# Kernel optimization log

Hardware: AMD Instinct MI355X
Metric: run time of the kernel (lower is better)

Reference implementation:

```python
import jax, jax.numpy as jnp
import numpy as np

B, D_IN, J = 65536, 512, 8
HIDDEN = [256, 128, 64]


def setup_inputs() -> dict:
    key = jax.random.key(0)
    ks = jax.random.split(key, 8)
    dims = [D_IN] + HIDDEN
    inp = {
        "x": jax.random.normal(ks[0], (B, D_IN), dtype=jnp.float32),
        # soft domain indicator (one-hot in practice; math is a weighted sum either way)
        "domain_indicator": jax.random.uniform(ks[1], (B, J), dtype=jnp.float32),
    }
    for i in range(3):
        fin, fout = dims[i], dims[i + 1]
        scale = (2.0 / (fin + fout)) ** 0.5  # glorot_normal
        inp[f"sk{i}"] = jax.random.normal(ks[2 + i], (fin, fout), dtype=jnp.float32) * scale
        inp[f"sb{i}"] = jnp.zeros((fout,), dtype=jnp.float32)
        inp[f"dk{i}"] = jax.random.normal(ks[5 + i], (J, fin, fout), dtype=jnp.float32) * scale
        inp[f"db{i}"] = jnp.zeros((J, fout), dtype=jnp.float32)
    return inp


def _star_forward(x, domain_indicator, layers):
    # layer 0: x is [B, D]; fused shared*domain weights -> batched per-domain GEMM
    sk, sb, dk, db = layers[0]
    w = sk[None] * dk                                   # [J, D, H0]
    h = jnp.einsum('bi,jio->bjo', x, w) + (sb[None] + db)[None]  # [B, J, H0]
    h = jax.nn.relu(h)
    for sk, sb, dk, db in layers[1:]:
        w = sk[None] * dk                               # [J, Hi, Hi+1]
        h = jnp.einsum('bji,jio->bjo', h, w) + (sb[None] + db)[None]
        h = jax.nn.relu(h)
    # select/mix domains: sum_j h[b,j,:] * indicator[b,j]
    return jnp.einsum('bjo,bj->bo', h, domain_indicator)


def reference(x, domain_indicator, sk0, sb0, dk0, db0, sk1, sb1, dk1, db1, sk2, sb2, dk2, db2):
    layers = [(sk0, sb0, dk0, db0), (sk1, sb1, dk1, db1), (sk2, sb2, dk2, db2)]
    return _star_forward(x, domain_indicator, layers)
```

## Files before the change

kernel.cpp:

```cpp
#include <hip/hip_runtime.h>
#include <stdint.h>


namespace {

typedef __attribute__((ext_vector_type(8))) short bf16x8;
typedef __attribute__((ext_vector_type(4))) float f32x4;

union Frag { bf16x8 v; unsigned int u[4]; };

constexpr size_t WS_L0   = 0;
constexpr size_t WS_L1   = 4194304;
constexpr size_t WS_L2   = 5242880;
constexpr size_t WS_B0   = 5505024;
constexpr size_t WS_B1   = 5513216;
constexpr size_t WS_B2   = 5517312;
constexpr size_t WS_X    = 5519360;
constexpr size_t WS_TOTAL_BIG = WS_X + (size_t)65536 * 2048;

constexpr int PREP_TOTAL = 1048576 + 262144 + 65536 + 2048 + 1024 + 512;
constexpr int XSPLIT_THREADS = 65536 * 64;

__device__ __forceinline__ void splitpair(float a, float b,
                                          unsigned int& hi, unsigned int& lo) {
    unsigned int ua = __float_as_uint(a);
    unsigned int ub = __float_as_uint(b);
    unsigned int ha = ua & 0xffff0000u;
    unsigned int hb = ub & 0xffff0000u;
    float ra = a - __uint_as_float(ha);
    float rb = b - __uint_as_float(hb);
    hi = (ua >> 16) | hb;
    lo = (__float_as_uint(ra) >> 16) | (__float_as_uint(rb) & 0xffff0000u);
}

__device__ __forceinline__ unsigned int packsplit(float v) {
    unsigned int u = __float_as_uint(v);
    unsigned int h = u & 0xffff0000u;
    float r = v - __uint_as_float(h);
    return h | (__float_as_uint(r) >> 16);
}

__device__ __forceinline__ void unpack2(unsigned int e0, unsigned int e1,
                                        unsigned int& hi, unsigned int& lo) {
    hi = (e0 >> 16) | (e1 & 0xffff0000u);
    lo = (e0 & 0xffffu) | (e1 << 16);
}

__device__ __forceinline__ void unpack2p(unsigned int e0, unsigned int e1,
                                         unsigned int& hi, unsigned int& lo) {
    hi = __builtin_amdgcn_perm(e1, e0, 0x07060302u);
    lo = __builtin_amdgcn_perm(e1, e0, 0x05040100u);
}

__device__ __forceinline__ unsigned int packsplitp(float v) {
    unsigned int u = __float_as_uint(v);
    float r = v - __uint_as_float(u & 0xffff0000u);
    return __builtin_amdgcn_perm(u, __float_as_uint(r), 0x07060302u);
}

__global__ void prep_ws(const float* __restrict__ sk0, const float* __restrict__ dk0,
                        const float* __restrict__ sk1, const float* __restrict__ dk1,
                        const float* __restrict__ sk2, const float* __restrict__ dk2,
                        const float* __restrict__ sb0, const float* __restrict__ db0,
                        const float* __restrict__ sb1, const float* __restrict__ db1,
                        const float* __restrict__ sb2, const float* __restrict__ db2,
                        char* __restrict__ ws) {
    int tid = blockIdx.x * 256 + threadIdx.x;
    if (tid < 1048576) {
        int n = tid & 255, k = (tid >> 8) & 511, j = tid >> 17;
        float wv = sk0[k * 256 + n] * dk0[(size_t)(j * 512 + k) * 256 + n];
        unsigned int u = __float_as_uint(wv);
        unsigned int h = u & 0xffff0000u;
        float r = wv - __uint_as_float(h);
        int pair = (j * 16 + (k >> 5)) * 16 + (n >> 4);
        int lane = (n & 15) | (((k >> 3) & 3) << 4);
        size_t off = WS_L0 + (size_t)pair * 2048 + lane * 16 + (k & 7) * 2;
        *(unsigned short*)(ws + off)        = (unsigned short)(u >> 16);
        *(unsigned short*)(ws + off + 1024) = (unsigned short)(__float_as_uint(r) >> 16);
    } else if (tid < 1310720) {
        int t = tid - 1048576;
        int n = t & 127, k = (t >> 7) & 255, j = t >> 15;
        float wv = sk1[k * 128 + n] * dk1[(size_t)(j * 256 + k) * 128 + n];
        unsigned int u = __float_as_uint(wv);
        unsigned int h = u & 0xffff0000u;
        float r = wv - __uint_as_float(h);
        int pair = (j * 8 + (k >> 5)) * 8 + (n >> 4);
        int lane = (n & 15) | (((k >> 3) & 3) << 4);
        size_t off = WS_L1 + (size_t)pair * 2048 + lane * 16 + (k & 7) * 2;
        *(unsigned short*)(ws + off)        = (unsigned short)(u >> 16);
        *(unsigned short*)(ws + off + 1024) = (unsigned short)(__float_as_uint(r) >> 16);
    } else if (tid < 1376256) {
        int t = tid - 1310720;
        int n = t & 63, k = (t >> 6) & 127, j = t >> 13;
        float wv = sk2[k * 64 + n] * dk2[(size_t)(j * 128 + k) * 64 + n];
        unsigned int u = __float_as_uint(wv);
        unsigned int h = u & 0xffff0000u;
        float r = wv - __uint_as_float(h);
        int pair = (j * 4 + (k >> 5)) * 4 + (n >> 4);
        int lane = (n & 15) | (((k >> 3) & 3) << 4);
        size_t off = WS_L2 + (size_t)pair * 2048 + lane * 16 + (k & 7) * 2;
        *(unsigned short*)(ws + off)        = (unsigned short)(u >> 16);
        *(unsigned short*)(ws + off + 1024) = (unsigned short)(__float_as_uint(r) >> 16);
    } else if (tid < 1378304) {
        int t = tid - 1376256;
        ((float*)(ws + WS_B0))[t] = sb0[t & 255] + db0[t];
    } else if (tid < 1379328) {
        int t = tid - 1378304;
        ((float*)(ws + WS_B1))[t] = sb1[t & 127] + db1[t];
    } else if (tid < PREP_TOTAL) {
        int t = tid - 1379328;
        ((float*)(ws + WS_B2))[t] = sb2[t & 63] + db2[t];
    }
}

__global__ void prep_xsplit(const float* __restrict__ x, char* __restrict__ ws) {
    int t = blockIdx.x * 256 + threadIdx.x;
    if (t >= XSPLIT_THREADS) return;
    const float4 a0 = *(const float4*)(x + (size_t)t * 8);
    const float4 a1 = *(const float4*)(x + (size_t)t * 8 + 4);
    unsigned int hi[4], lo[4];
    splitpair(a0.x, a0.y, hi[0], lo[0]);
    splitpair(a0.z, a0.w, hi[1], lo[1]);
    splitpair(a1.x, a1.y, hi[2], lo[2]);
    splitpair(a1.z, a1.w, hi[3], lo[3]);
    char* dst = ws + WS_X + (size_t)t * 32;
    *(uint4*)dst        = *(uint4*)hi;
    *(uint4*)(dst + 16) = *(uint4*)lo;
}

__global__ __launch_bounds__(512, 4) void star_mfma_v3(
    const float* __restrict__ ind,
    const char* __restrict__ ws,
    float* __restrict__ out)
{
    __shared__ unsigned int H0s[32 * 260];
    __shared__ unsigned int H1s[32 * 132];
    __shared__ float indS[8 * 33];

    const int tid  = threadIdx.x;
    const int w    = tid >> 6;
    const int lane = tid & 63;
    const int c    = lane & 15;
    const int q    = lane >> 4;
    const int b0   = blockIdx.x * 32;
    const int mt2  = w >> 2;
    const int nt2  = w & 3;

    const char* xp  = ws + WS_X;
    const char* wB0 = ws + WS_L0;
    const char* wB1 = ws + WS_L1;
    const char* wB2 = ws + WS_L2;
    const float* bias0 = (const float*)(ws + WS_B0);
    const float* bias1 = (const float*)(ws + WS_B1);
    const float* bias2 = (const float*)(ws + WS_B2);

    if (tid < 256) indS[(tid & 7) * 33 + (tid >> 3)] = ind[(size_t)b0 * 8 + tid];

    const f32x4 z = {0.f, 0.f, 0.f, 0.f};
    f32x4 oacc = z;

    __syncthreads();

    for (int jp = 0; jp < 2; ++jp) {
        f32x4 acc0[4][2][2];
#pragma unroll
        for (int jj = 0; jj < 4; ++jj)
#pragma unroll
            for (int mt = 0; mt < 2; ++mt)
#pragma unroll
                for (int ntl = 0; ntl < 2; ++ntl) acc0[jj][mt][ntl] = z;

        for (int kc = 0; kc < 16; ++kc) {
            Frag Ahi[2], Alo[2];
#pragma unroll
            for (int mt = 0; mt < 2; ++mt) {
                const char* ap = xp + (size_t)(b0 + mt * 16 + c) * 2048 + (kc * 4 + q) * 32;
                *(uint4*)Ahi[mt].u = *(const uint4*)ap;
                *(uint4*)Alo[mt].u = *(const uint4*)(ap + 16);
            }
#pragma unroll
            for (int jj = 0; jj < 4; ++jj) {
                const int j = jp * 4 + jj;
#pragma unroll
                for (int ntl = 0; ntl < 2; ++ntl) {
                    const int nt = w * 2 + ntl;
                    const char* pb = wB0 + ((size_t)((j * 16 + kc) * 16 + nt) * 2048) + lane * 16;
                    Frag Bhi, Blo;
                    *(uint4*)Bhi.u = *(const uint4*)pb;
                    *(uint4*)Blo.u = *(const uint4*)(pb + 1024);
#pragma unroll
                    for (int mt = 0; mt < 2; ++mt) {
                        acc0[jj][mt][ntl] = __builtin_amdgcn_mfma_f32_16x16x32_bf16(Ahi[mt].v, Bhi.v, acc0[jj][mt][ntl], 0, 0, 0);
                        acc0[jj][mt][ntl] = __builtin_amdgcn_mfma_f32_16x16x32_bf16(Ahi[mt].v, Blo.v, acc0[jj][mt][ntl], 0, 0, 0);
                        acc0[jj][mt][ntl] = __builtin_amdgcn_mfma_f32_16x16x32_bf16(Alo[mt].v, Bhi.v, acc0[jj][mt][ntl], 0, 0, 0);
                    }
                }
            }
        }

#pragma unroll
        for (int jj = 0; jj < 4; ++jj) {
            const int j = jp * 4 + jj;

#pragma unroll
            for (int ntl = 0; ntl < 2; ++ntl) {
                const float bv = bias0[j * 256 + w * 32 + ntl * 16 + c];
#pragma unroll
                for (int mt = 0; mt < 2; ++mt)
#pragma unroll
                    for (int r = 0; r < 4; ++r) {
                        float v = fmaxf(acc0[jj][mt][ntl][r] + bv, 0.f);
                        H0s[(mt * 16 + q * 4 + r) * 260 + w * 32 + ntl * 16 + c] = packsplitp(v);
                    }
            }
            __syncthreads();

            f32x4 acc1[2]; acc1[0] = z; acc1[1] = z;
            for (int kc = 0; kc < 8; ++kc) {
                Frag Ahi[2], Alo[2];
#pragma unroll
                for (int mt = 0; mt < 2; ++mt) {
                    const unsigned int* hp = &H0s[(mt * 16 + c) * 260 + kc * 32 + q * 8];
                    uint4 e0 = *(const uint4*)hp;
                    uint4 e1 = *(const uint4*)(hp + 4);
                    unpack2p(e0.x, e0.y, Ahi[mt].u[0], Alo[mt].u[0]);
                    unpack2p(e0.z, e0.w, Ahi[mt].u[1], Alo[mt].u[1]);
                    unpack2p(e1.x, e1.y, Ahi[mt].u[2], Alo[mt].u[2]);
                    unpack2p(e1.z, e1.w, Ahi[mt].u[3], Alo[mt].u[3]);
                }
                const char* pb = wB1 + ((size_t)((j * 8 + kc) * 8 + w) * 2048) + lane * 16;
                Frag Bhi, Blo;
                *(uint4*)Bhi.u = *(const uint4*)pb;
                *(uint4*)Blo.u = *(const uint4*)(pb + 1024);
#pragma unroll
                for (int mt = 0; mt < 2; ++mt) {
                    acc1[mt] = __builtin_amdgcn_mfma_f32_16x16x32_bf16(Ahi[mt].v, Bhi.v, acc1[mt], 0, 0, 0);
                    acc1[mt] = __builtin_amdgcn_mfma_f32_16x16x32_bf16(Ahi[mt].v, Blo.v, acc1[mt], 0, 0, 0);
                    acc1[mt] = __builtin_amdgcn_mfma_f32_16x16x32_bf16(Alo[mt].v, Bhi.v, acc1[mt], 0, 0, 0);
                }
            }
            {
                const float bv = bias1[j * 128 + w * 16 + c];
#pragma unroll
                for (int mt = 0; mt < 2; ++mt)
#pragma unroll
                    for (int r = 0; r < 4; ++r) {
                        float v = fmaxf(acc1[mt][r] + bv, 0.f);
                        H1s[(mt * 16 + q * 4 + r) * 132 + w * 16 + c] = packsplitp(v);
                    }
            }
            __syncthreads();

            f32x4 acc2 = z;
            for (int kc = 0; kc < 4; ++kc) {
                Frag Ahi, Alo;
                const unsigned int* hp = &H1s[(mt2 * 16 + c) * 132 + kc * 32 + q * 8];
                uint4 e0 = *(const uint4*)hp;
                uint4 e1 = *(const uint4*)(hp + 4);
                unpack2p(e0.x, e0.y, Ahi.u[0], Alo.u[0]);
                unpack2p(e0.z, e0.w, Ahi.u[1], Alo.u[1]);
                unpack2p(e1.x, e1.y, Ahi.u[2], Alo.u[2]);
                unpack2p(e1.z, e1.w, Ahi.u[3], Alo.u[3]);
                const char* pb = wB2 + ((size_t)((j * 4 + kc) * 4 + nt2) * 2048) + lane * 16;
                Frag Bhi, Blo;
                *(uint4*)Bhi.u = *(const uint4*)pb;
                *(uint4*)Blo.u = *(const uint4*)(pb + 1024);
                acc2 = __builtin_amdgcn_mfma_f32_16x16x32_bf16(Ahi.v, Bhi.v, acc2, 0, 0, 0);
                acc2 = __builtin_amdgcn_mfma_f32_16x16x32_bf16(Ahi.v, Blo.v, acc2, 0, 0, 0);
                acc2 = __builtin_amdgcn_mfma_f32_16x16x32_bf16(Alo.v, Bhi.v, acc2, 0, 0, 0);
            }
            {
                const float bv = bias2[j * 64 + nt2 * 16 + c];
#pragma unroll
                for (int r = 0; r < 4; ++r) {
                    float v = fmaxf(acc2[r] + bv, 0.f);
                    oacc[r] = fmaf(indS[j * 33 + mt2 * 16 + q * 4 + r], v, oacc[r]);
                }
            }
        }
    }

#pragma unroll
    for (int r = 0; r < 4; ++r)
        out[(size_t)(b0 + mt2 * 16 + q * 4 + r) * 64 + nt2 * 16 + c] = oacc[r];
}

__global__ __launch_bounds__(256, 3) void star_mfma_fb(
    const float* __restrict__ x,
    const float* __restrict__ ind,
    const char* __restrict__ ws,
    float* __restrict__ out)
{
    __shared__ unsigned int H0s[32 * 260];
    __shared__ unsigned int H1s[32 * 132];
    __shared__ float indS[8 * 33];

    const int tid  = threadIdx.x;
    const int w    = tid >> 6;
    const int lane = tid & 63;
    const int c    = lane & 15;
    const int q    = lane >> 4;
    const int b0   = blockIdx.x * 32;

    const char* wB0 = ws + WS_L0;
    const char* wB1 = ws + WS_L1;
    const char* wB2 = ws + WS_L2;
    const float* bias0 = (const float*)(ws + WS_B0);
    const float* bias1 = (const float*)(ws + WS_B1);
    const float* bias2 = (const float*)(ws + WS_B2);

    indS[(tid & 7) * 33 + (tid >> 3)] = ind[(size_t)b0 * 8 + tid];

    const f32x4 z = {0.f, 0.f, 0.f, 0.f};
    f32x4 oacc[2]; oacc[0] = z; oacc[1] = z;

    __syncthreads();

    for (int j = 0; j < 8; ++j) {
        f32x4 acc0[2][4];
#pragma unroll
        for (int mt = 0; mt < 2; ++mt)
#pragma unroll
            for (int ntl = 0; ntl < 4; ++ntl) acc0[mt][ntl] = z;

        for (int kc = 0; kc < 16; ++kc) {
            Frag Ahi[2], Alo[2];
#pragma unroll
            for (int mt = 0; mt < 2; ++mt) {
                const float* ap = x + (size_t)(b0 + mt * 16 + c) * 512 + kc * 32 + q * 8;
                float4 a0 = *(const float4*)ap;
                float4 a1 = *(const float4*)(ap + 4);
                splitpair(a0.x, a0.y, Ahi[mt].u[0], Alo[mt].u[0]);
                splitpair(a0.z, a0.w, Ahi[mt].u[1], Alo[mt].u[1]);
                splitpair(a1.x, a1.y, Ahi[mt].u[2], Alo[mt].u[2]);
                splitpair(a1.z, a1.w, Ahi[mt].u[3], Alo[mt].u[3]);
            }
#pragma unroll
            for (int ntl = 0; ntl < 4; ++ntl) {
                const int nt = w * 4 + ntl;
                const char* pb = wB0 + ((size_t)((j * 16 + kc) * 16 + nt) * 2048) + lane * 16;
                Frag Bhi, Blo;
                *(uint4*)Bhi.u = *(const uint4*)pb;
                *(uint4*)Blo.u = *(const uint4*)(pb + 1024);
#pragma unroll
                for (int mt = 0; mt < 2; ++mt) {
                    acc0[mt][ntl] = __builtin_amdgcn_mfma_f32_16x16x32_bf16(Ahi[mt].v, Bhi.v, acc0[mt][ntl], 0, 0, 0);
                    acc0[mt][ntl] = __builtin_amdgcn_mfma_f32_16x16x32_bf16(Ahi[mt].v, Blo.v, acc0[mt][ntl], 0, 0, 0);
                    acc0[mt][ntl] = __builtin_amdgcn_mfma_f32_16x16x32_bf16(Alo[mt].v, Bhi.v, acc0[mt][ntl], 0, 0, 0);
                }
            }
        }
#pragma unroll
        for (int ntl = 0; ntl < 4; ++ntl) {
            const float bv = bias0[j * 256 + w * 64 + ntl * 16 + c];
#pragma unroll
            for (int mt = 0; mt < 2; ++mt)
#pragma unroll
                for (int r = 0; r < 4; ++r) {
                    float v = acc0[mt][ntl][r] + bv;
                    v = fmaxf(v, 0.f);
                    H0s[(mt * 16 + q * 4 + r) * 260 + w * 64 + ntl * 16 + c] = packsplit(v);
                }
        }
        __syncthreads();

        f32x4 acc1[2][2];
#pragma unroll
        for (int mt = 0; mt < 2; ++mt)
#pragma unroll
            for (int ntl = 0; ntl < 2; ++ntl) acc1[mt][ntl] = z;

        for (int kc = 0; kc < 8; ++kc) {
            Frag Ahi[2], Alo[2];
#pragma unroll
            for (int mt = 0; mt < 2; ++mt) {
                const unsigned int* hp = &H0s[(mt * 16 + c) * 260 + kc * 32 + q * 8];
                uint4 e0 = *(const uint4*)hp;
                uint4 e1 = *(const uint4*)(hp + 4);
                unpack2(e0.x, e0.y, Ahi[mt].u[0], Alo[mt].u[0]);
                unpack2(e0.z, e0.w, Ahi[mt].u[1], Alo[mt].u[1]);
                unpack2(e1.x, e1.y, Ahi[mt].u[2], Alo[mt].u[2]);
                unpack2(e1.z, e1.w, Ahi[mt].u[3], Alo[mt].u[3]);
            }
#pragma unroll
            for (int ntl = 0; ntl < 2; ++ntl) {
                const int nt = w * 2 + ntl;
                const char* pb = wB1 + ((size_t)((j * 8 + kc) * 8 + nt) * 2048) + lane * 16;
                Frag Bhi, Blo;
                *(uint4*)Bhi.u = *(const uint4*)pb;
                *(uint4*)Blo.u = *(const uint4*)(pb + 1024);
#pragma unroll
                for (int mt = 0; mt < 2; ++mt) {
                    acc1[mt][ntl] = __builtin_amdgcn_mfma_f32_16x16x32_bf16(Ahi[mt].v, Bhi.v, acc1[mt][ntl], 0, 0, 0);
                    acc1[mt][ntl] = __builtin_amdgcn_mfma_f32_16x16x32_bf16(Ahi[mt].v, Blo.v, acc1[mt][ntl], 0, 0, 0);
                    acc1[mt][ntl] = __builtin_amdgcn_mfma_f32_16x16x32_bf16(Alo[mt].v, Bhi.v, acc1[mt][ntl], 0, 0, 0);
                }
            }
        }
#pragma unroll
        for (int ntl = 0; ntl < 2; ++ntl) {
            const float bv = bias1[j * 128 + w * 32 + ntl * 16 + c];
#pragma unroll
            for (int mt = 0; mt < 2; ++mt)
#pragma unroll
                for (int r = 0; r < 4; ++r) {
                    float v = acc1[mt][ntl][r] + bv;
                    v = fmaxf(v, 0.f);
                    H1s[(mt * 16 + q * 4 + r) * 132 + w * 32 + ntl * 16 + c] = packsplit(v);
                }
        }
        __syncthreads();

        f32x4 acc2[2]; acc2[0] = z; acc2[1] = z;

        for (int kc = 0; kc < 4; ++kc) {
            Frag Ahi[2], Alo[2];
#pragma unroll
            for (int mt = 0; mt < 2; ++mt) {
                const unsigned int* hp = &H1s[(mt * 16 + c) * 132 + kc * 32 + q * 8];
                uint4 e0 = *(const uint4*)hp;
                uint4 e1 = *(const uint4*)(hp + 4);
                unpack2(e0.x, e0.y, Ahi[mt].u[0], Alo[mt].u[0]);
                unpack2(e0.z, e0.w, Ahi[mt].u[1], Alo[mt].u[1]);
                unpack2(e1.x, e1.y, Ahi[mt].u[2], Alo[mt].u[2]);
                unpack2(e1.z, e1.w, Ahi[mt].u[3], Alo[mt].u[3]);
            }
            const char* pb = wB2 + ((size_t)((j * 4 + kc) * 4 + w) * 2048) + lane * 16;
            Frag Bhi, Blo;
            *(uint4*)Bhi.u = *(const uint4*)pb;
            *(uint4*)Blo.u = *(const uint4*)(pb + 1024);
#pragma unroll
            for (int mt = 0; mt < 2; ++mt) {
                acc2[mt] = __builtin_amdgcn_mfma_f32_16x16x32_bf16(Ahi[mt].v, Bhi.v, acc2[mt], 0, 0, 0);
                acc2[mt] = __builtin_amdgcn_mfma_f32_16x16x32_bf16(Ahi[mt].v, Blo.v, acc2[mt], 0, 0, 0);
                acc2[mt] = __builtin_amdgcn_mfma_f32_16x16x32_bf16(Alo[mt].v, Bhi.v, acc2[mt], 0, 0, 0);
            }
        }
        {
            const float bv = bias2[j * 64 + w * 16 + c];
#pragma unroll
            for (int mt = 0; mt < 2; ++mt)
#pragma unroll
                for (int r = 0; r < 4; ++r) {
                    float v = acc2[mt][r] + bv;
                    v = fmaxf(v, 0.f);
                    oacc[mt][r] = fmaf(indS[j * 33 + mt * 16 + q * 4 + r], v, oacc[mt][r]);
                }
        }
    }

#pragma unroll
    for (int mt = 0; mt < 2; ++mt)
#pragma unroll
        for (int r = 0; r < 4; ++r)
            out[(size_t)(b0 + mt * 16 + q * 4 + r) * 64 + w * 16 + c] = oacc[mt][r];
}

}

extern "C" void kernel_launch(void* const* d_in, const int* in_sizes, int n_in,
                              void* d_out, int out_size, void* d_ws, size_t ws_size,
                              hipStream_t stream) {
    const float* x   = (const float*)d_in[0];
    const float* ind = (const float*)d_in[1];
    const float* sk0 = (const float*)d_in[2];
    const float* sb0 = (const float*)d_in[3];
    const float* dk0 = (const float*)d_in[4];
    const float* db0 = (const float*)d_in[5];
    const float* sk1 = (const float*)d_in[6];
    const float* sb1 = (const float*)d_in[7];
    const float* dk1 = (const float*)d_in[8];
    const float* db1 = (const float*)d_in[9];
    const float* sk2 = (const float*)d_in[10];
    const float* sb2 = (const float*)d_in[11];
    const float* dk2 = (const float*)d_in[12];
    const float* db2 = (const float*)d_in[13];
    char* ws   = (char*)d_ws;
    float* out = (float*)d_out;

    prep_ws<<<dim3((PREP_TOTAL + 255) / 256), dim3(256), 0, stream>>>(
        sk0, dk0, sk1, dk1, sk2, dk2, sb0, db0, sb1, db1, sb2, db2, ws);

    if (ws_size >= WS_TOTAL_BIG) {
        prep_xsplit<<<dim3(XSPLIT_THREADS / 256), dim3(256), 0, stream>>>(x, ws);
        star_mfma_v3<<<dim3(2048), dim3(512), 0, stream>>>(ind, ws, out);
    } else {
        star_mfma_fb<<<dim3(2048), dim3(256), 0, stream>>>(x, ind, ws, out);
    }
}
```

Before: 918.7 us.

## Store split x in MFMA fragment order and split hi/lo LDS planes

The x prep kernel now goes through shared memory to write the bf16 hi/lo split in MFMA lane-fragment order, with hi and lo halves 1024 bytes apart. Each wave's A-fragment global load is then one contiguous 1 KB read instead of a strided row gather. The intermediate activations in LDS are stored as separate hi and lo bf16 planes rather than packed 32-bit words, so fragment reads become direct 16-byte loads with no perm unpacking. In exchange, the epilogue does twice as many 16-bit LDS stores, and the prep kernel adds an LDS transpose.

```diff
diff --git a/kernel.cpp b/kernel.cpp
--- a/kernel.cpp
+++ b/kernel.cpp
@@ -19,7 +19,6 @@
 constexpr size_t WS_TOTAL_BIG = WS_X + (size_t)65536 * 2048;
 
 constexpr int PREP_TOTAL = 1048576 + 262144 + 65536 + 2048 + 1024 + 512;
-constexpr int XSPLIT_THREADS = 65536 * 64;
 
 __device__ __forceinline__ void splitpair(float a, float b,
                                           unsigned int& hi, unsigned int& lo) {
@@ -33,6 +32,13 @@
     lo = (__float_as_uint(ra) >> 16) | (__float_as_uint(rb) & 0xffff0000u);
 }
 
+__device__ __forceinline__ void split16(float v, unsigned short& h, unsigned short& l) {
+    unsigned int u = __float_as_uint(v);
+    h = (unsigned short)(u >> 16);
+    float r = v - __uint_as_float(u & 0xffff0000u);
+    l = (unsigned short)(__float_as_uint(r) >> 16);
+}
+
 __device__ __forceinline__ unsigned int packsplit(float v) {
     unsigned int u = __float_as_uint(v);
     unsigned int h = u & 0xffff0000u;
@@ -44,18 +50,6 @@
                                         unsigned int& hi, unsigned int& lo) {
     hi = (e0 >> 16) | (e1 & 0xffff0000u);
     lo = (e0 & 0xffffu) | (e1 << 16);
-}
-
-__device__ __forceinline__ void unpack2p(unsigned int e0, unsigned int e1,
-                                         unsigned int& hi, unsigned int& lo) {
-    hi = __builtin_amdgcn_perm(e1, e0, 0x07060302u);
-    lo = __builtin_amdgcn_perm(e1, e0, 0x05040100u);
-}
-
-__device__ __forceinline__ unsigned int packsplitp(float v) {
-    unsigned int u = __float_as_uint(v);
-    float r = v - __uint_as_float(u & 0xffff0000u);
-    return __builtin_amdgcn_perm(u, __float_as_uint(r), 0x07060302u);
 }
 
 __global__ void prep_ws(const float* __restrict__ sk0, const float* __restrict__ dk0,
@@ -113,28 +107,50 @@
     }
 }
 
-__global__ void prep_xsplit(const float* __restrict__ x, char* __restrict__ ws) {
-    int t = blockIdx.x * 256 + threadIdx.x;
-    if (t >= XSPLIT_THREADS) return;
-    const float4 a0 = *(const float4*)(x + (size_t)t * 8);
-    const float4 a1 = *(const float4*)(x + (size_t)t * 8 + 4);
-    unsigned int hi[4], lo[4];
-    splitpair(a0.x, a0.y, hi[0], lo[0]);
-    splitpair(a0.z, a0.w, hi[1], lo[1]);
-    splitpair(a1.x, a1.y, hi[2], lo[2]);
-    splitpair(a1.z, a1.w, hi[3], lo[3]);
-    char* dst = ws + WS_X + (size_t)t * 32;
-    *(uint4*)dst        = *(uint4*)hi;
-    *(uint4*)(dst + 16) = *(uint4*)lo;
-}
-
-__global__ __launch_bounds__(512, 4) void star_mfma_v3(
+__global__ __launch_bounds__(256) void prep_xsplit(const float* __restrict__ x,
+                                                   char* __restrict__ ws) {
+    __shared__ __align__(16) unsigned int xf[8192];
+    const int b     = blockIdx.x;
+    const int tid   = threadIdx.x;
+    const int row16 = tid >> 4;
+    const int seg   = tid & 15;
+
+    const float* src = x + ((size_t)b * 16 + row16) * 512 + seg * 32;
+    float4 a[8];
+#pragma unroll
+    for (int i = 0; i < 8; ++i) a[i] = *(const float4*)(src + i * 4);
+
+    unsigned int hi[16], lo[16];
+#pragma unroll
+    for (int i = 0; i < 8; ++i) {
+        splitpair(a[i].x, a[i].y, hi[2 * i],     lo[2 * i]);
+        splitpair(a[i].z, a[i].w, hi[2 * i + 1], lo[2 * i + 1]);
+    }
+#pragma unroll
+    for (int qq = 0; qq < 4; ++qq) {
+        const int lane = row16 | (qq << 4);
+        const int di = seg * 512 + lane * 4;
+        uint4 vh = { hi[qq * 4 + 0], hi[qq * 4 + 1], hi[qq * 4 + 2], hi[qq * 4 + 3] };
+        uint4 vl = { lo[qq * 4 + 0], lo[qq * 4 + 1], lo[qq * 4 + 2], lo[qq * 4 + 3] };
+        *(uint4*)&xf[di]       = vh;
+        *(uint4*)&xf[di + 256] = vl;
+    }
+    __syncthreads();
+
+    uint4* dst = (uint4*)(ws + WS_X + (size_t)b * 32768) + tid * 8;
+#pragma unroll
+    for (int i = 0; i < 8; ++i) dst[i] = *(const uint4*)&xf[tid * 32 + i * 4];
+}
+
+__global__ __launch_bounds__(512, 4) void star_mfma_v5(
     const float* __restrict__ ind,
     const char* __restrict__ ws,
     float* __restrict__ out)
 {
-    __shared__ unsigned int H0s[32 * 260];
-    __shared__ unsigned int H1s[32 * 132];
+    __shared__ __align__(16) unsigned short H0hi[32 * 264];
+    __shared__ __align__(16) unsigned short H0lo[32 * 264];
+    __shared__ __align__(16) unsigned short H1hi[32 * 136];
+    __shared__ __align__(16) unsigned short H1lo[32 * 136];
     __shared__ float indS[8 * 33];
 
     const int tid  = threadIdx.x;
@@ -174,9 +190,9 @@
             Frag Ahi[2], Alo[2];
 #pragma unroll
             for (int mt = 0; mt < 2; ++mt) {
-                const char* ap = xp + (size_t)(b0 + mt * 16 + c) * 2048 + (kc * 4 + q) * 32;
+                const char* ap = xp + ((size_t)((blockIdx.x * 2 + mt) * 16 + kc) * 2048) + lane * 16;
                 *(uint4*)Ahi[mt].u = *(const uint4*)ap;
-                *(uint4*)Alo[mt].u = *(const uint4*)(ap + 16);
+                *(uint4*)Alo[mt].u = *(const uint4*)(ap + 1024);
             }
 #pragma unroll
             for (int jj = 0; jj < 4; ++jj) {
@@ -204,13 +220,18 @@
 
 #pragma unroll
             for (int ntl = 0; ntl < 2; ++ntl) {
-                const float bv = bias0[j * 256 + w * 32 + ntl * 16 + c];
+                const int k = w * 32 + ntl * 16 + c;
+                const float bv = bias0[j * 256 + k];
 #pragma unroll
                 for (int mt = 0; mt < 2; ++mt)
 #pragma unroll
                     for (int r = 0; r < 4; ++r) {
                         float v = fmaxf(acc0[jj][mt][ntl][r] + bv, 0.f);
-                        H0s[(mt * 16 + q * 4 + r) * 260 + w * 32 + ntl * 16 + c] = packsplitp(v);
+                        unsigned short h16, l16;
+                        split16(v, h16, l16);
+                        const int idx = (mt * 16 + q * 4 + r) * 264 + k;
+                        H0hi[idx] = h16;
+                        H0lo[idx] = l16;
                     }
             }
             __syncthreads();
@@ -220,13 +241,9 @@
                 Frag Ahi[2], Alo[2];
 #pragma unroll
                 for (int mt = 0; mt < 2; ++mt) {
-                    const unsigned int* hp = &H0s[(mt * 16 + c) * 260 + kc * 32 + q * 8];
-                    uint4 e0 = *(const uint4*)hp;
-                    uint4 e1 = *(const uint4*)(hp + 4);
-                    unpack2p(e0.x, e0.y, Ahi[mt].u[0], Alo[mt].u[0]);
-                    unpack2p(e0.z, e0.w, Ahi[mt].u[1], Alo[mt].u[1]);
-                    unpack2p(e1.x, e1.y, Ahi[mt].u[2], Alo[mt].u[2]);
-                    unpack2p(e1.z, e1.w, Ahi[mt].u[3], Alo[mt].u[3]);
+                    const int idx = (mt * 16 + c) * 264 + kc * 32 + q * 8;
+                    *(uint4*)Ahi[mt].u = *(const uint4*)&H0hi[idx];
+                    *(uint4*)Alo[mt].u = *(const uint4*)&H0lo[idx];
                 }
                 const char* pb = wB1 + ((size_t)((j * 8 + kc) * 8 + w) * 2048) + lane * 16;
                 Frag Bhi, Blo;
@@ -240,13 +257,18 @@
                 }
             }
             {
-                const float bv = bias1[j * 128 + w * 16 + c];
+                const int k = w * 16 + c;
+                const float bv = bias1[j * 128 + k];
 #pragma unroll
                 for (int mt = 0; mt < 2; ++mt)
 #pragma unroll
                     for (int r = 0; r < 4; ++r) {
                         float v = fmaxf(acc1[mt][r] + bv, 0.f);
-                        H1s[(mt * 16 + q * 4 + r) * 132 + w * 16 + c] = packsplitp(v);
+                        unsigned short h16, l16;
+                        split16(v, h16, l16);
+                        const int idx = (mt * 16 + q * 4 + r) * 136 + k;
+                        H1hi[idx] = h16;
+                        H1lo[idx] = l16;
                     }
             }
             __syncthreads();
@@ -254,13 +276,9 @@
             f32x4 acc2 = z;
             for (int kc = 0; kc < 4; ++kc) {
                 Frag Ahi, Alo;
-                const unsigned int* hp = &H1s[(mt2 * 16 + c) * 132 + kc * 32 + q * 8];
-                uint4 e0 = *(const uint4*)hp;
-                uint4 e1 = *(const uint4*)(hp + 4);
-                unpack2p(e0.x, e0.y, Ahi.u[0], Alo.u[0]);
-                unpack2p(e0.z, e0.w, Ahi.u[1], Alo.u[1]);
-                unpack2p(e1.x, e1.y, Ahi.u[2], Alo.u[2]);
-                unpack2p(e1.z, e1.w, Ahi.u[3], Alo.u[3]);
+                const int idx = (mt2 * 16 + c) * 136 + kc * 32 + q * 8;
+                *(uint4*)Ahi.u = *(const uint4*)&H1hi[idx];
+                *(uint4*)Alo.u = *(const uint4*)&H1lo[idx];
                 const char* pb = wB2 + ((size_t)((j * 4 + kc) * 4 + nt2) * 2048) + lane * 16;
                 Frag Bhi, Blo;
                 *(uint4*)Bhi.u = *(const uint4*)pb;
@@ -482,8 +500,8 @@
         sk0, dk0, sk1, dk1, sk2, dk2, sb0, db0, sb1, db1, sb2, db2, ws);
 
     if (ws_size >= WS_TOTAL_BIG) {
-        prep_xsplit<<<dim3(XSPLIT_THREADS / 256), dim3(256), 0, stream>>>(x, ws);
-        star_mfma_v3<<<dim3(2048), dim3(512), 0, stream>>>(ind, ws, out);
+        prep_xsplit<<<dim3(4096), dim3(256), 0, stream>>>(x, ws);
+        star_mfma_v5<<<dim3(2048), dim3(512), 0, stream>>>(ind, ws, out);
     } else {
         star_mfma_fb<<<dim3(2048), dim3(256), 0, stream>>>(x, ind, ws, out);
     }
```

Result: faster. 848.2 us (-7.7%).
